# Optimization experiments

Hardware: AMD Instinct MI355X
Metric: run time of the kernel (lower is better)

## Reference

```python
import jax, jax.numpy as jnp
import numpy as np

B, SQ, SK = 2, 2048, 2048
QDIM = KDIM = HID = 1024
H = 16
DH = HID // H  # inner_dim = 64


def setup_inputs() -> dict:
    key = jax.random.key(0)
    ks = jax.random.split(key, 8)
    q = jax.random.normal(ks[0], (B, SQ, QDIM), dtype=jnp.float32)
    k = jax.random.normal(ks[1], (B, SK, KDIM), dtype=jnp.float32)
    v = jax.random.normal(ks[2], (B, SK, KDIM), dtype=jnp.float32)
    mask = jax.random.randint(ks[3], (B, SQ, SK), 0, 2).astype(jnp.bool_)
    scale = 1.0 / np.sqrt(QDIM)
    # per-head projections, stored stacked: [H, in_dim, DH]
    Wq = jax.random.normal(ks[4], (H, QDIM, DH), dtype=jnp.float32) * scale
    Wk = jax.random.normal(ks[5], (H, KDIM, DH), dtype=jnp.float32) * scale
    Wv = jax.random.normal(ks[6], (H, KDIM, DH), dtype=jnp.float32) * scale
    Wo = jax.random.normal(ks[7], (HID, QDIM), dtype=jnp.float32) * scale
    return {"q": q, "k": k, "v": v, "mask": mask,
            "Wq": Wq, "Wk": Wk, "Wv": Wv, "Wo": Wo}


def reference(q, k, v, mask, Wq, Wk, Wv, Wo):
    dh = Wq.shape[-1]
    qh = jnp.einsum('bsd,hde->bhse', q, Wq)   # [B,H,SQ,DH]
    kh = jnp.einsum('bsd,hde->bhse', k, Wk)   # [B,H,SK,DH]
    vh = jnp.einsum('bsd,hde->bhse', v, Wv)   # [B,H,SK,DH]
    scores = jnp.einsum('bhqd,bhkd->bhqk', qh, kh) / jnp.sqrt(jnp.asarray(dh, qh.dtype))
    scores = jnp.where(mask[:, None, :, :], -jnp.inf, scores)
    attn = jax.nn.softmax(scores, axis=-1)
    att = jnp.einsum('bhqk,bhkd->bhqd', attn, vh)        # [B,H,SQ,DH]
    concat = att.transpose(0, 2, 1, 3).reshape(q.shape[0], q.shape[1], -1)  # head-order concat
    return concat @ Wo  # [B,SQ,QDIM]
```

## Files before the change

kernel.cpp:

```cpp
#include <hip/hip_runtime.h>

#define NB 2
#define NH 16
#define SEQ 2048
#define DMODEL 1024
#define DHEAD 64
#define QSCALE 0.18033688f

typedef __attribute__((ext_vector_type(8))) short bf16x8;
typedef __attribute__((ext_vector_type(4))) short bf16x4;
typedef __attribute__((ext_vector_type(4))) float f32x4;
typedef __attribute__((ext_vector_type(16))) float f32x16;
typedef __attribute__((ext_vector_type(4))) int i32x4;

static __device__ __forceinline__ unsigned short f2bf(float f) {
    unsigned int u = __float_as_uint(f);
    u += 0x7fffu + ((u >> 16) & 1u);
    return (unsigned short)(u >> 16);
}
static __device__ __forceinline__ unsigned int pk2(float lo, float hi) {
    return (unsigned int)f2bf(lo) | ((unsigned int)f2bf(hi) << 16);
}
static __device__ __forceinline__ void gld_lds16(const unsigned short* g, unsigned short* l) {
    __builtin_amdgcn_global_load_lds(
        (const __attribute__((address_space(1))) unsigned int*)g,
        (__attribute__((address_space(3))) unsigned int*)l, 16, 0, 0);
}

__global__ __launch_bounds__(256) void prep_kernel(
    const int* __restrict__ mask, unsigned long long* __restrict__ mpack,
    const float* __restrict__ Wq, const float* __restrict__ Wk, const float* __restrict__ Wv,
    unsigned short* __restrict__ Wqt, unsigned short* __restrict__ Wkt,
    unsigned short* __restrict__ Wvt,
    const float* __restrict__ Wo, unsigned short* __restrict__ Wot,
    const float* __restrict__ q, const float* __restrict__ k, const float* __restrict__ v,
    unsigned short* __restrict__ qb, unsigned short* __restrict__ kb,
    unsigned short* __restrict__ vb)
{
    __shared__ __align__(16) float Ls[64][65];
    const int bid = blockIdx.x, t = threadIdx.x;

    if (bid < 1024) {
        const int wave = bid * 4 + (t >> 6);
        const int lane = t & 63;
        const int* row = mask + (size_t)wave * SEQ;
        unsigned long long* orow = mpack + (size_t)wave * (SEQ / 64);
        for (int w = 0; w < SEQ / 64; ++w) {
            int m = row[w * 64 + lane];
            unsigned long long bits = __ballot(m != 0);
            if (lane == 0) orow[w] = bits;
        }
    } else if (bid < 2048) {
        const float* S; unsigned short* D; float scale; int R, tile_r, tile_c, ostride;
        if (bid < 1792) {
            const int local = bid - 1024, z = local >> 4, sel = z >> 4, h = z & 15;
            S = (sel == 0 ? Wq : sel == 1 ? Wk : Wv) + (size_t)h * DMODEL * DHEAD;
            D = (sel == 0 ? Wqt : sel == 1 ? Wkt : Wvt) + (size_t)h * DMODEL * DHEAD;
            scale = (sel == 0) ? QSCALE : 1.0f;
            tile_r = (local & 15) * 64; tile_c = 0; R = DHEAD; ostride = DMODEL;
        } else {
            const int local = bid - 1792;
            S = Wo; D = Wot; scale = 1.0f;
            tile_c = (local & 15) * 64; tile_r = (local >> 4) * 64; R = DMODEL; ostride = DMODEL;
        }
        const int c4 = (t & 15) * 4;
        for (int rr = t >> 4; rr < 64; rr += 16) {
            float4 x = *(const float4*)(S + (size_t)(tile_r + rr) * R + tile_c + c4);
            Ls[rr][c4 + 0] = x.x; Ls[rr][c4 + 1] = x.y;
            Ls[rr][c4 + 2] = x.z; Ls[rr][c4 + 3] = x.w;
        }
        __syncthreads();
        const int r4 = (t & 15) * 4;
        for (int cc = t >> 4; cc < 64; cc += 16) {
            ushort4 o;
            o.x = f2bf(Ls[r4 + 0][cc] * scale); o.y = f2bf(Ls[r4 + 1][cc] * scale);
            o.z = f2bf(Ls[r4 + 2][cc] * scale); o.w = f2bf(Ls[r4 + 3][cc] * scale);
            *(ushort4*)(D + (size_t)(tile_c + cc) * ostride + tile_r + r4) = o;
        }
    } else {
        const int local = bid - 2048;
        const int z = local >> 11;
        const float* S = (z == 0) ? q : (z == 1) ? k : v;
        unsigned short* D = (z == 0) ? qb : (z == 1) ? kb : vb;
        const size_t i = ((size_t)(local & 2047) * 256 + t) * 8;
        float4 x0 = *(const float4*)(S + i);
        float4 x1 = *(const float4*)(S + i + 4);
        uint4 val;
        val.x = pk2(x0.x, x0.y); val.y = pk2(x0.z, x0.w);
        val.z = pk2(x1.x, x1.y); val.w = pk2(x1.z, x1.w);
        *(uint4*)(D + i) = val;
    }
}

__global__ __launch_bounds__(256) void proj_gemm_kernel(
    const unsigned short* __restrict__ qb, const unsigned short* __restrict__ kb,
    const unsigned short* __restrict__ vb,
    const unsigned short* __restrict__ Wqt, const unsigned short* __restrict__ Wkt,
    const unsigned short* __restrict__ Wvt,
    unsigned short* __restrict__ qh, unsigned short* __restrict__ kh,
    unsigned short* __restrict__ vt)
{
    const int bid = blockIdx.x;
    const int sx = bid >> 3;
    const int mtg = (bid & 7) * 12 + (sx >> 3);
    const int z = mtg >> 5;
    const int m0 = (mtg & 31) * 128;
    const int n0 = (sx & 7) * 128;

    const unsigned short* A = (z == 0) ? qb : (z == 1) ? kb : vb;
    const unsigned short* Bt = (z == 0) ? Wqt : (z == 1) ? Wkt : Wvt;

    const int t = threadIdx.x, lane = t & 63, w = t >> 6;
    const int lg = lane >> 4, ln = lane & 15;
    const int wx = w & 1, wy = w >> 1;

    __shared__ __align__(16) unsigned short SM[17408];
    unsigned short* As = SM;
    unsigned short* Bs = SM + 8192;

    f32x4 acc[4][4] = {};

    for (int kk = 0; kk < DMODEL; kk += 64) {
        #pragma unroll
        for (int i = 0; i < 4; ++i) {
            int s = (w * 4 + i) * 64 + lane;
            int n = s >> 3, c = (s & 7) ^ (n & 7);
            gld_lds16(Bt + (size_t)(n0 + n) * DMODEL + kk + c * 8, Bs + (size_t)s * 8);
        }
        #pragma unroll
        for (int i = 0; i < 4; ++i) {
            int s = (w * 4 + i) * 64 + lane;
            int n = s >> 3, c = (s & 7) ^ (n & 7);
            gld_lds16(A + (size_t)(m0 + n) * DMODEL + kk + c * 8, As + (size_t)s * 8);
        }
        __syncthreads();
        #pragma unroll
        for (int ks = 0; ks < 2; ++ks) {
            bf16x8 af[4], bf[4];
            #pragma unroll
            for (int rb = 0; rb < 4; ++rb) {
                int r = wy * 64 + rb * 16 + ln;
                af[rb] = *(const bf16x8*)(As + r * 64 + (((ks * 4 + lg) ^ (r & 7)) * 8));
            }
            #pragma unroll
            for (int nb = 0; nb < 4; ++nb) {
                int n = wx * 64 + nb * 16 + ln;
                bf[nb] = *(const bf16x8*)(Bs + n * 64 + (((ks * 4 + lg) ^ (n & 7)) * 8));
            }
            #pragma unroll
            for (int rb = 0; rb < 4; ++rb)
                #pragma unroll
                for (int nb = 0; nb < 4; ++nb)
                    acc[rb][nb] = __builtin_amdgcn_mfma_f32_16x16x32_bf16(
                        af[rb], bf[nb], acc[rb][nb], 0, 0, 0);
        }
        __syncthreads();
    }

    if (z < 2) {
        unsigned short* Y = (z == 0) ? qh : kh;
        unsigned short* Ep = SM;
        #pragma unroll
        for (int rb = 0; rb < 4; ++rb)
            #pragma unroll
            for (int nb = 0; nb < 4; ++nb) {
                const int c_l = wx * 64 + nb * 16 + ln;
                const int base = ((c_l >> 6) << 13) + (c_l & 63);
                #pragma unroll
                for (int r = 0; r < 4; ++r) {
                    const int s_l = wy * 64 + rb * 16 + lg * 4 + r;
                    Ep[base + s_l * 64] = f2bf(acc[rb][nb][r]);
                }
            }
        __syncthreads();
        {
            const int head = t >> 7, r2 = t & 127;
            const unsigned short* src = Ep + head * 8192 + r2 * 64;
            unsigned short* dst = Y + ((size_t)((m0 >> 11) * NH + (n0 >> 6) + head) * SEQ
                                       + (m0 & (SEQ - 1)) + r2) * DHEAD;
            #pragma unroll
            for (int i = 0; i < 8; ++i)
                *(uint4*)(dst + i * 8) = *(const uint4*)(src + i * 8);
        }
    } else {
        unsigned short* Ep = SM;
        #pragma unroll
        for (int rb = 0; rb < 4; ++rb)
            #pragma unroll
            for (int nb = 0; nb < 4; ++nb) {
                const int c_l = wx * 64 + nb * 16 + ln;
                const int seq0 = wy * 64 + rb * 16 + lg * 4;
                ushort4 o;
                o.x = f2bf(acc[rb][nb][0]); o.y = f2bf(acc[rb][nb][1]);
                o.z = f2bf(acc[rb][nb][2]); o.w = f2bf(acc[rb][nb][3]);
                *(ushort4*)(Ep + (c_l >> 6) * 8704 + (c_l & 63) * 136 + seq0) = o;
            }
        __syncthreads();
        {
            const int head = t >> 7, dh = (t >> 1) & 63, hf = t & 1;
            const unsigned short* src = Ep + head * 8704 + dh * 136 + hf * 64;
            unsigned short* dst = vt
                + ((size_t)((((m0 >> 11) << 4) + (n0 >> 6) + head) * DHEAD + dh) * SEQ
                   + (m0 & (SEQ - 1)) + hf * 64);
            #pragma unroll
            for (int i = 0; i < 8; ++i)
                *(uint4*)(dst + i * 8) = *(const uint4*)(src + i * 8);
        }
    }
}

__global__ __launch_bounds__(256, 2) void attn_kernel(
    const unsigned short* __restrict__ qh, const unsigned short* __restrict__ kh,
    const unsigned short* __restrict__ vt, const unsigned long long* __restrict__ mpack,
    unsigned short* __restrict__ att)
{
    const int t = threadIdx.x, lane = t & 63, w = t >> 6;
    const int h = lane >> 5, lq = lane & 31;
    const int L = lq & 7, X = (lq >> 3) & 3;

    const int bid = blockIdx.x;
    const int r_ = bid >> 3;
    const int qt = r_ & 15;
    const int bh = (bid & 7) * 4 + (r_ >> 4);
    const int b = bh >> 4, hd = bh & 15;
    const int row0 = qt * 128;
    const int qrow = row0 + w * 32 + lq;

    __shared__ __align__(16) unsigned short SMEM[4 * 8192];

    const unsigned short* Kb = kh + (size_t)bh * SEQ * DHEAD;
    const unsigned short* Vb = vt + (size_t)bh * DHEAD * SEQ;

    const unsigned short* Qb = qh + ((size_t)bh * SEQ + qrow) * DHEAD;
    bf16x8 qf[4];
    #pragma unroll
    for (int d = 0; d < 4; ++d) qf[d] = *(const bf16x8*)(Qb + d * 16 + h * 8);

    const unsigned long long* Mb = mpack + ((size_t)b * SEQ + qrow) * (SEQ / 64);

    int oK[4], oV[4], sL[4];
    #pragma unroll
    for (int i = 0; i < 4; ++i) {
        const int s = i * 256 + t;
        sL[i] = s * 8;
        { const int n = s >> 3, c = (s & 7) ^ (n & 7) ^ ((n >> 3) & 3);
          oK[i] = n * DHEAD + c * 8; }
        { const int n = s >> 4, c = (s & 15) ^ (n & 7) ^ ((n >> 3) & 3);
          oV[i] = n * SEQ + c * 8; }
    }

    f32x16 acc[2] = {};
    f32x16 lacc = {};
    bf16x8 ones;
    #pragma unroll
    for (int i = 0; i < 8; ++i) ones[i] = (short)0x3f80;

    ulonglong2 mw, mwn;

    #pragma unroll
    for (int i = 0; i < 4; ++i)
        gld_lds16(Kb + oK[i], SMEM + sL[i]);
    #pragma unroll
    for (int i = 0; i < 4; ++i)
        gld_lds16(Vb + oV[i], SMEM + 16384 + sL[i]);
    mw = *(const ulonglong2*)(Mb);
    __syncthreads();

    for (int tix = 0; tix < 16; ++tix) {
        const int buf = tix & 1;

        if (tix < 15) {
            const int ktn = (tix + 1) * 128;
            unsigned short* Kd = SMEM + (buf ^ 1) * 8192;
            unsigned short* Vd = SMEM + 16384 + (buf ^ 1) * 8192;
            #pragma unroll
            for (int i = 0; i < 4; ++i)
                gld_lds16(Kb + (size_t)ktn * DHEAD + oK[i], Kd + sL[i]);
            #pragma unroll
            for (int i = 0; i < 4; ++i)
                gld_lds16(Vb + (size_t)ktn + oV[i], Vd + sL[i]);
            mwn = *(const ulonglong2*)(Mb + (size_t)(tix + 1) * 2);
        }

        const unsigned short* Ksb = SMEM + buf * 8192;
        const unsigned short* Vsb = SMEM + 16384 + buf * 8192;
        const unsigned long long mh0 = mw.x >> (h * 4);
        const unsigned long long mh1 = mw.y >> (h * 4);

        #pragma unroll
        for (int st = 0; st < 4; ++st) {
            f32x16 S = {};
            #pragma unroll
            for (int d = 0; d < 4; ++d) {
                bf16x8 kf = *(const bf16x8*)(Ksb + (st * 32 + lq) * 64
                                             + (((d * 2 + h) ^ L ^ X) * 8));
                S = __builtin_amdgcn_mfma_f32_32x32x16_bf16(kf, qf[d], S, 0, 0, 0);
            }
            const unsigned long long mh = (st < 2) ? mh0 : mh1;
            const int sb = 32 * (st & 1);
            unsigned int pd[8];
            #pragma unroll
            for (int bb = 0; bb < 4; ++bb) {
                float e[4];
                #pragma unroll
                for (int rr = 0; rr < 4; ++rr) {
                    const bool m = (mh >> (sb + 8 * bb + rr)) & 1ull;
                    float ex = __builtin_amdgcn_exp2f(S[bb * 4 + rr]);
                    e[rr] = m ? 0.0f : ex;
                }
                pd[bb * 2 + 0] = __builtin_amdgcn_perm(
                    __float_as_uint(e[1]), __float_as_uint(e[0]), 0x07060302u);
                pd[bb * 2 + 1] = __builtin_amdgcn_perm(
                    __float_as_uint(e[3]), __float_as_uint(e[2]), 0x07060302u);
            }
            #pragma unroll
            for (int k2 = 0; k2 < 2; ++k2) {
                i32x4 pi = { (int)pd[4 * k2 + 0], (int)pd[4 * k2 + 1],
                             (int)pd[4 * k2 + 2], (int)pd[4 * k2 + 3] };
                bf16x8 pf = __builtin_bit_cast(bf16x8, pi);
                lacc = __builtin_amdgcn_mfma_f32_32x32x16_bf16(ones, pf, lacc, 0, 0, 0);
                const int p0 = (((4 * st + 2 * k2) ^ L ^ X)) * 8;
                #pragma unroll
                for (int dt = 0; dt < 2; ++dt) {
                    const unsigned short* vb_ = Vsb + (dt * 32 + lq) * 128 + 4 * h;
                    bf16x4 v0 = *(const bf16x4*)(vb_ + p0);
                    bf16x4 v1 = *(const bf16x4*)(vb_ + (p0 ^ 8));
                    bf16x8 vf = __builtin_shufflevector(v0, v1, 0, 1, 2, 3, 4, 5, 6, 7);
                    acc[dt] = __builtin_amdgcn_mfma_f32_32x32x16_bf16(vf, pf, acc[dt], 0, 0, 0);
                }
            }
        }

        mw = mwn;
        __syncthreads();
    }

    const float linv = 1.0f / lacc[0];
    unsigned short* Ar = att + ((size_t)b * SEQ + qrow) * DMODEL + hd * DHEAD;
    #pragma unroll
    for (int dt = 0; dt < 2; ++dt)
        #pragma unroll
        for (int g = 0; g < 4; ++g) {
            const int dh0 = dt * 32 + 8 * g + 4 * h;
            ushort4 o;
            o.x = f2bf(acc[dt][g * 4 + 0] * linv);
            o.y = f2bf(acc[dt][g * 4 + 1] * linv);
            o.z = f2bf(acc[dt][g * 4 + 2] * linv);
            o.w = f2bf(acc[dt][g * 4 + 3] * linv);
            *(ushort4*)(Ar + dh0) = o;
        }
}

__global__ __launch_bounds__(256) void out_gemm_kernel(
    const unsigned short* __restrict__ A, const unsigned short* __restrict__ Bt,
    float* __restrict__ C)
{
    const int bid = blockIdx.x;
    const int sx = bid >> 3;
    const int m0 = ((bid & 7) * 8 + (sx >> 3)) * 64;
    const int n0 = (sx & 7) * 128;

    const int t = threadIdx.x, lane = t & 63, w = t >> 6;
    const int lg = lane >> 4, ln = lane & 15;
    const int wx = w & 1, wy = w >> 1;

    __shared__ __align__(16) unsigned short As[64 * 64];
    __shared__ __align__(16) unsigned short Bs[128 * 64];

    f32x4 acc[2][4] = {};

    for (int kk = 0; kk < DMODEL; kk += 64) {
        #pragma unroll
        for (int i = 0; i < 4; ++i) {
            int s = (w * 4 + i) * 64 + lane;
            int n = s >> 3, c = (s & 7) ^ (n & 7);
            gld_lds16(Bt + (size_t)(n0 + n) * DMODEL + kk + c * 8, Bs + (size_t)s * 8);
        }
        #pragma unroll
        for (int i = 0; i < 2; ++i) {
            int s = (w * 2 + i) * 64 + lane;
            int n = s >> 3, c = (s & 7) ^ (n & 7);
            gld_lds16(A + (size_t)(m0 + n) * DMODEL + kk + c * 8, As + (size_t)s * 8);
        }
        __syncthreads();
        #pragma unroll
        for (int ks = 0; ks < 2; ++ks) {
            bf16x8 af[2], bf[4];
            #pragma unroll
            for (int rb = 0; rb < 2; ++rb) {
                int r = wy * 32 + rb * 16 + ln;
                af[rb] = *(const bf16x8*)(As + r * 64 + (((ks * 4 + lg) ^ (r & 7)) * 8));
            }
            #pragma unroll
            for (int nb = 0; nb < 4; ++nb) {
                int n = wx * 64 + nb * 16 + ln;
                bf[nb] = *(const bf16x8*)(Bs + n * 64 + (((ks * 4 + lg) ^ (n & 7)) * 8));
            }
            #pragma unroll
            for (int rb = 0; rb < 2; ++rb)
                #pragma unroll
                for (int nb = 0; nb < 4; ++nb)
                    acc[rb][nb] = __builtin_amdgcn_mfma_f32_16x16x32_bf16(
                        af[rb], bf[nb], acc[rb][nb], 0, 0, 0);
        }
        __syncthreads();
    }

    #pragma unroll
    for (int rb = 0; rb < 2; ++rb)
        #pragma unroll
        for (int nb = 0; nb < 4; ++nb)
            #pragma unroll
            for (int r = 0; r < 4; ++r) {
                int grow = m0 + wy * 32 + rb * 16 + lg * 4 + r;
                int gcol = n0 + wx * 64 + nb * 16 + ln;
                C[(size_t)grow * DMODEL + gcol] = acc[rb][nb][r];
            }
}

extern "C" void kernel_launch(void* const* d_in, const int* in_sizes, int n_in,
                              void* d_out, int out_size, void* d_ws, size_t ws_size,
                              hipStream_t stream) {
    const float* q    = (const float*)d_in[0];
    const float* k    = (const float*)d_in[1];
    const float* v    = (const float*)d_in[2];
    const int*   mask = (const int*)  d_in[3];
    const float* Wq   = (const float*)d_in[4];
    const float* Wk   = (const float*)d_in[5];
    const float* Wv   = (const float*)d_in[6];
    const float* Wo   = (const float*)d_in[7];
    float* out = (float*)d_out;

    unsigned short* ws  = (unsigned short*)d_ws;
    const size_t n1 = (size_t)NB * NH * SEQ * DHEAD;
    const size_t nw = (size_t)NH * DHEAD * DMODEL;
    unsigned short* qh  = ws;
    unsigned short* kh  = qh + n1;
    unsigned short* vt  = kh + n1;
    unsigned short* att = vt + n1;
    unsigned short* Wqt = att + n1;
    unsigned short* Wkt = Wqt + nw;
    unsigned short* Wvt = Wkt + nw;
    unsigned short* Wot = Wvt + nw;
    unsigned long long* mpack = (unsigned long long*)(Wot + nw);
    unsigned short* regA = (unsigned short*)(mpack + (size_t)NB * SEQ * (SEQ / 64));
    unsigned short* qb = regA;
    unsigned short* kb = qb + n1;
    unsigned short* vb = kb + n1;

    prep_kernel<<<dim3(8192), 256, 0, stream>>>(
        mask, mpack, Wq, Wk, Wv, Wqt, Wkt, Wvt, Wo, Wot, q, k, v, qb, kb, vb);
    proj_gemm_kernel<<<dim3(768), 256, 0, stream>>>(qb, kb, vb, Wqt, Wkt, Wvt, qh, kh, vt);
    attn_kernel<<<dim3(512), 256, 0, stream>>>(qh, kh, vt, mpack, att);
    out_gemm_kernel<<<dim3(512), 256, 0, stream>>>(att, Wot, out);
}
```

Baseline: 254.2 us.

## Split attention KV range across two wave groups per block with LDS reduction

Attention blocks grow to 512 threads. Each half of the block processes half of the key sequence, using 64-key tiles, its own double-buffered K/V LDS region and its own mask word. At the end the second half writes its partial output and row sums to LDS, and the first half combines them and normalizes. The aim is more waves per CU and more latency hiding without changing the grid size. In exchange it adds an LDS reduction, a final sync, and smaller tiles that give less work per barrier.

Result: no change. 254.4 us (+0.1%).

```diff
diff --git a/kernel.cpp b/kernel.cpp
--- a/kernel.cpp
+++ b/kernel.cpp
@@ -209,12 +209,15 @@
     }
 }
 
-__global__ __launch_bounds__(256, 2) void attn_kernel(
+__global__ __launch_bounds__(512, 4) void attn_kernel(
     const unsigned short* __restrict__ qh, const unsigned short* __restrict__ kh,
     const unsigned short* __restrict__ vt, const unsigned long long* __restrict__ mpack,
     unsigned short* __restrict__ att)
 {
-    const int t = threadIdx.x, lane = t & 63, w = t >> 6;
+    const int t = threadIdx.x, lane = t & 63;
+    const int w8 = t >> 6;
+    const int half = w8 >> 2, w = w8 & 3;
+    const int th = t & 255;
     const int h = lane >> 5, lq = lane & 31;
     const int L = lq & 7, X = (lq >> 3) & 3;
 
@@ -225,8 +228,11 @@
     const int b = bh >> 4, hd = bh & 15;
     const int row0 = qt * 128;
     const int qrow = row0 + w * 32 + lq;
-
-    __shared__ __align__(16) unsigned short SMEM[4 * 8192];
+    const int kt0 = half * (SEQ / 2);
+
+    __shared__ __align__(16) unsigned short SMEM[2 * 16384];
+    unsigned short* Kh = SMEM + half * 16384;
+    unsigned short* Vh = Kh + 8192;
 
     const unsigned short* Kb = kh + (size_t)bh * SEQ * DHEAD;
     const unsigned short* Vb = vt + (size_t)bh * DHEAD * SEQ;
@@ -238,15 +244,14 @@
 
     const unsigned long long* Mb = mpack + ((size_t)b * SEQ + qrow) * (SEQ / 64);
 
-    int oK[4], oV[4], sL[4];
-    #pragma unroll
-    for (int i = 0; i < 4; ++i) {
-        const int s = i * 256 + t;
+    int oK[2], oV[2], sL[2];
+    #pragma unroll
+    for (int i = 0; i < 2; ++i) {
+        const int s = i * 256 + th;
+        const int n = s >> 3, c = (s & 7) ^ (n & 7) ^ ((n >> 3) & 3);
         sL[i] = s * 8;
-        { const int n = s >> 3, c = (s & 7) ^ (n & 7) ^ ((n >> 3) & 3);
-          oK[i] = n * DHEAD + c * 8; }
-        { const int n = s >> 4, c = (s & 15) ^ (n & 7) ^ ((n >> 3) & 3);
-          oV[i] = n * SEQ + c * 8; }
+        oK[i] = n * DHEAD + c * 8;
+        oV[i] = n * SEQ + c * 8;
     }
 
     f32x16 acc[2] = {};
@@ -255,40 +260,39 @@
     #pragma unroll
     for (int i = 0; i < 8; ++i) ones[i] = (short)0x3f80;
 
-    ulonglong2 mw, mwn;
-
-    #pragma unroll
-    for (int i = 0; i < 4; ++i)
-        gld_lds16(Kb + oK[i], SMEM + sL[i]);
-    #pragma unroll
-    for (int i = 0; i < 4; ++i)
-        gld_lds16(Vb + oV[i], SMEM + 16384 + sL[i]);
-    mw = *(const ulonglong2*)(Mb);
+    unsigned long long mw, mwn = 0;
+
+    #pragma unroll
+    for (int i = 0; i < 2; ++i)
+        gld_lds16(Kb + (size_t)kt0 * DHEAD + oK[i], Kh + sL[i]);
+    #pragma unroll
+    for (int i = 0; i < 2; ++i)
+        gld_lds16(Vb + (size_t)kt0 + oV[i], Vh + sL[i]);
+    mw = Mb[half << 4];
     __syncthreads();
 
     for (int tix = 0; tix < 16; ++tix) {
         const int buf = tix & 1;
 
         if (tix < 15) {
-            const int ktn = (tix + 1) * 128;
-            unsigned short* Kd = SMEM + (buf ^ 1) * 8192;
-            unsigned short* Vd = SMEM + 16384 + (buf ^ 1) * 8192;
-            #pragma unroll
-            for (int i = 0; i < 4; ++i)
+            const int ktn = kt0 + (tix + 1) * 64;
+            unsigned short* Kd = Kh + (buf ^ 1) * 4096;
+            unsigned short* Vd = Vh + (buf ^ 1) * 4096;
+            #pragma unroll
+            for (int i = 0; i < 2; ++i)
                 gld_lds16(Kb + (size_t)ktn * DHEAD + oK[i], Kd + sL[i]);
             #pragma unroll
-            for (int i = 0; i < 4; ++i)
+            for (int i = 0; i < 2; ++i)
                 gld_lds16(Vb + (size_t)ktn + oV[i], Vd + sL[i]);
-            mwn = *(const ulonglong2*)(Mb + (size_t)(tix + 1) * 2);
-        }
-
-        const unsigned short* Ksb = SMEM + buf * 8192;
-        const unsigned short* Vsb = SMEM + 16384 + buf * 8192;
-        const unsigned long long mh0 = mw.x >> (h * 4);
-        const unsigned long long mh1 = mw.y >> (h * 4);
-
-        #pragma unroll
-        for (int st = 0; st < 4; ++st) {
+            mwn = Mb[(half << 4) + tix + 1];
+        }
+
+        const unsigned short* Ksb = Kh + buf * 4096;
+        const unsigned short* Vsb = Vh + buf * 4096;
+        const unsigned long long mh_ = mw >> (h * 4);
+
+        #pragma unroll
+        for (int st = 0; st < 2; ++st) {
             f32x16 S = {};
             #pragma unroll
             for (int d = 0; d < 4; ++d) {
@@ -296,15 +300,14 @@
                                              + (((d * 2 + h) ^ L ^ X) * 8));
                 S = __builtin_amdgcn_mfma_f32_32x32x16_bf16(kf, qf[d], S, 0, 0, 0);
             }
-            const unsigned long long mh = (st < 2) ? mh0 : mh1;
-            const int sb = 32 * (st & 1);
+            const int sb = 32 * st;
             unsigned int pd[8];
             #pragma unroll
             for (int bb = 0; bb < 4; ++bb) {
                 float e[4];
                 #pragma unroll
                 for (int rr = 0; rr < 4; ++rr) {
-                    const bool m = (mh >> (sb + 8 * bb + rr)) & 1ull;
+                    const bool m = (mh_ >> (sb + 8 * bb + rr)) & 1ull;
                     float ex = __builtin_amdgcn_exp2f(S[bb * 4 + rr]);
                     e[rr] = m ? 0.0f : ex;
                 }
@@ -322,7 +325,7 @@
                 const int p0 = (((4 * st + 2 * k2) ^ L ^ X)) * 8;
                 #pragma unroll
                 for (int dt = 0; dt < 2; ++dt) {
-                    const unsigned short* vb_ = Vsb + (dt * 32 + lq) * 128 + 4 * h;
+                    const unsigned short* vb_ = Vsb + (dt * 32 + lq) * 64 + 4 * h;
                     bf16x4 v0 = *(const bf16x4*)(vb_ + p0);
                     bf16x4 v1 = *(const bf16x4*)(vb_ + (p0 ^ 8));
                     bf16x8 vf = __builtin_shufflevector(v0, v1, 0, 1, 2, 3, 4, 5, 6, 7);
@@ -335,20 +338,39 @@
         __syncthreads();
     }
 
-    const float linv = 1.0f / lacc[0];
-    unsigned short* Ar = att + ((size_t)b * SEQ + qrow) * DMODEL + hd * DHEAD;
-    #pragma unroll
-    for (int dt = 0; dt < 2; ++dt)
-        #pragma unroll
-        for (int g = 0; g < 4; ++g) {
-            const int dh0 = dt * 32 + 8 * g + 4 * h;
-            ushort4 o;
-            o.x = f2bf(acc[dt][g * 4 + 0] * linv);
-            o.y = f2bf(acc[dt][g * 4 + 1] * linv);
-            o.z = f2bf(acc[dt][g * 4 + 2] * linv);
-            o.w = f2bf(acc[dt][g * 4 + 3] * linv);
-            *(ushort4*)(Ar + dh0) = o;
-        }
+    const int rloc = w * 32 + lq;
+    float* Osh = (float*)SMEM;
+    float* Lsh = (float*)SMEM + 128 * 68;
+
+    if (half == 1) {
+        #pragma unroll
+        for (int dt = 0; dt < 2; ++dt)
+            #pragma unroll
+            for (int g = 0; g < 4; ++g) {
+                f32x4 v = { acc[dt][g * 4 + 0], acc[dt][g * 4 + 1],
+                            acc[dt][g * 4 + 2], acc[dt][g * 4 + 3] };
+                *(f32x4*)(Osh + rloc * 68 + dt * 32 + 8 * g + 4 * h) = v;
+            }
+        if (h == 0) Lsh[rloc] = lacc[0];
+    }
+    __syncthreads();
+    if (half == 0) {
+        const float linv = 1.0f / (lacc[0] + Lsh[rloc]);
+        unsigned short* Ar = att + ((size_t)b * SEQ + qrow) * DMODEL + hd * DHEAD;
+        #pragma unroll
+        for (int dt = 0; dt < 2; ++dt)
+            #pragma unroll
+            for (int g = 0; g < 4; ++g) {
+                const int dh0 = dt * 32 + 8 * g + 4 * h;
+                f32x4 p = *(const f32x4*)(Osh + rloc * 68 + dh0);
+                ushort4 o;
+                o.x = f2bf((acc[dt][g * 4 + 0] + p[0]) * linv);
+                o.y = f2bf((acc[dt][g * 4 + 1] + p[1]) * linv);
+                o.z = f2bf((acc[dt][g * 4 + 2] + p[2]) * linv);
+                o.w = f2bf((acc[dt][g * 4 + 3] + p[3]) * linv);
+                *(ushort4*)(Ar + dh0) = o;
+            }
+    }
 }
 
 __global__ __launch_bounds__(256) void out_gemm_kernel(
@@ -451,6 +473,6 @@
     prep_kernel<<<dim3(8192), 256, 0, stream>>>(
         mask, mpack, Wq, Wk, Wv, Wqt, Wkt, Wvt, Wo, Wot, q, k, v, qb, kb, vb);
     proj_gemm_kernel<<<dim3(768), 256, 0, stream>>>(qb, kb, vb, Wqt, Wkt, Wvt, qh, kh, vt);
-    attn_kernel<<<dim3(512), 256, 0, stream>>>(qh, kh, vt, mpack, att);
+    attn_kernel<<<dim3(512), 512, 0, stream>>>(qh, kh, vt, mpack, att);
     out_gemm_kernel<<<dim3(512), 256, 0, stream>>>(att, Wot, out);
 }
```
